# Performance work log

Hardware: AMD Instinct MI355X
Metric: run time of the kernel (lower is better)

Reference implementation:

```python
import jax, jax.numpy as jnp
import numpy as np

EMB = 1024
HEADS = 16
HEAD_DIM = EMB // HEADS
D_FF = 4 * EMB
EPS = 1e-5


def setup_inputs() -> dict:
    key = jax.random.key(0)
    ks = jax.random.split(key, 12)
    b, t = 4, 2048
    sc = 0.02
    return {
        "x": jax.random.normal(ks[0], (b, t, EMB), dtype=jnp.float32),
        # weights stored [in, out] (transpose of torch Linear.weight)
        "w_attn": jax.random.normal(ks[1], (EMB, 3 * EMB), dtype=jnp.float32) * sc,
        "b_attn": jnp.zeros((3 * EMB,), dtype=jnp.float32),
        "w_proj": jax.random.normal(ks[2], (EMB, EMB), dtype=jnp.float32) * sc,
        "b_proj": jnp.zeros((EMB,), dtype=jnp.float32),
        "ln1_g": jnp.ones((EMB,), dtype=jnp.float32),
        "ln1_b": jnp.zeros((EMB,), dtype=jnp.float32),
        "w_ff1": jax.random.normal(ks[3], (EMB, D_FF), dtype=jnp.float32) * sc,
        "b_ff1": jnp.zeros((D_FF,), dtype=jnp.float32),
        "w_ff2": jax.random.normal(ks[4], (D_FF, EMB), dtype=jnp.float32) * sc,
        "b_ff2": jnp.zeros((EMB,), dtype=jnp.float32),
        "ln2_g": jnp.ones((EMB,), dtype=jnp.float32),
        "ln2_b": jnp.zeros((EMB,), dtype=jnp.float32),
    }


def _layernorm(x, g, b):
    mu = jnp.mean(x, axis=-1, keepdims=True)
    var = jnp.var(x, axis=-1, keepdims=True)
    return (x - mu) * jax.lax.rsqrt(var + EPS) * g + b


def reference(x, w_attn, b_attn, w_proj, b_proj, ln1_g, ln1_b,
              w_ff1, b_ff1, w_ff2, b_ff2, ln2_g, ln2_b):
    b, t, e = x.shape
    h, s = HEADS, HEAD_DIM
    # fused qkv projection (GPT2-style c_attn)
    qkv = x @ w_attn + b_attn                      # [b, t, 3e]
    q, k, v = jnp.split(qkv, 3, axis=-1)
    q = q.reshape(b, t, h, s).transpose(0, 2, 1, 3)  # [b, h, t, s]
    k = k.reshape(b, t, h, s).transpose(0, 2, 1, 3)
    v = v.reshape(b, t, h, s).transpose(0, 2, 1, 3)
    dot = jnp.einsum('bhqs,bhks->bhqk', q, k) / jnp.sqrt(jnp.float32(s))
    # causal mask: mask_(..., mask_diagonal=False) zeroes i < j (strict upper)
    causal = jnp.tril(jnp.ones((t, t), dtype=bool))
    dot = jnp.where(causal, dot, jnp.float32(-jnp.inf))
    att = jax.nn.softmax(dot, axis=-1)
    out = jnp.einsum('bhqk,bhks->bhqs', att, v)    # [b, h, t, s]
    out = out.transpose(0, 2, 1, 3).reshape(b, t, e)
    attended = out @ w_proj + b_proj
    # residual + LayerNorm (dropout is identity in eval mode)
    x1 = _layernorm(attended + x, ln1_g, ln1_b)
    ff = jax.nn.relu(x1 @ w_ff1 + b_ff1) @ w_ff2 + b_ff2
    return _layernorm(ff + x1, ln2_g, ln2_b)
```

## Files before the change

### kernel.cpp

```cpp
#include <hip/hip_runtime.h>
#include <hip/hip_bf16.h>


typedef __attribute__((ext_vector_type(8))) short bf16x8;
typedef __attribute__((ext_vector_type(4))) float f32x4;

__device__ __forceinline__ float b2f(unsigned short u) {
  return __uint_as_float(((unsigned int)u) << 16);
}
__device__ __forceinline__ unsigned short f2b(float f) {
  unsigned int u = __float_as_uint(f);
  u += 0x7fffu + ((u >> 16) & 1u);
  return (unsigned short)(u >> 16);
}
__device__ __forceinline__ unsigned int pk2b(float a, float b) {
  __hip_bfloat162 h = __float22bfloat162_rn(make_float2(a, b));
  return *(unsigned int*)&h;
}
__device__ __forceinline__ void gload_lds16(const unsigned short* g, unsigned short* l) {
  __builtin_amdgcn_global_load_lds((const __attribute__((address_space(1))) void*)g,
                                   (__attribute__((address_space(3))) void*)l, 16, 0, 0);
}

__global__ __launch_bounds__(256) void cvt_bf16(const float* __restrict__ in,
                                                unsigned short* __restrict__ out, long n) {
  long i = ((long)blockIdx.x * 256 + threadIdx.x) * 4;
  if (i >= n) return;
  float4 v = *(const float4*)(in + i);
  *(ushort4*)(out + i) = make_ushort4(f2b(v.x), f2b(v.y), f2b(v.z), f2b(v.w));
}

__global__ __launch_bounds__(256) void transpose_bf16(const float* __restrict__ in,
                                                      unsigned short* __restrict__ out,
                                                      int R, int C) {
  __shared__ float tile[32][33];
  int c0 = blockIdx.x * 32, r0 = blockIdx.y * 32;
  for (int i = threadIdx.y; i < 32; i += 8)
    tile[i][threadIdx.x] = in[(long)(r0 + i) * C + c0 + threadIdx.x];
  __syncthreads();
  for (int i = threadIdx.y; i < 32; i += 8)
    out[(long)(c0 + i) * R + r0 + threadIdx.x] = f2b(tile[threadIdx.x][i]);
}

template <int EPI>
__global__ __launch_bounds__(256) void gemm_bf16(const unsigned short* __restrict__ A,
                                                 const unsigned short* __restrict__ Bt,
                                                 const float* __restrict__ bias,
                                                 void* __restrict__ Cout,
                                                 void* __restrict__ Cout2,
                                                 int M, int N, int K, int Kstride) {
  __shared__ unsigned short As[128 * 32];
  __shared__ unsigned short Bs[128 * 32];
  int t = threadIdx.x;
  int bm = blockIdx.x * 128, bn = blockIdx.y * 128;
  int chunk = blockIdx.z;
  int w = t >> 6, lane = t & 63;
  int wr = w >> 1, wc = w & 1, quad = lane >> 4, l16 = lane & 15;
  int srow = t >> 2, scol = (t & 3) * 8;

  const unsigned short* Ap = A + (long)(bm + srow) * Kstride + (long)chunk * K + scol;
  const unsigned short* Bp = Bt + (long)(bn + srow) * Kstride + (long)chunk * K + scol;
  unsigned short* Asw = As + w * 512;
  unsigned short* Bsw = Bs + w * 512;

  f32x4 acc[4][4] = {};

  for (int k0 = 0; k0 < K; k0 += 32) {
    __syncthreads();
    gload_lds16(Ap + k0, Asw);
    gload_lds16(Ap + (long)64 * Kstride + k0, Asw + 2048);
    gload_lds16(Bp + k0, Bsw);
    gload_lds16(Bp + (long)64 * Kstride + k0, Bsw + 2048);
    __syncthreads();
    bf16x8 af[4], bfr[4];
#pragma unroll
    for (int i = 0; i < 4; ++i)
      af[i] = *(const bf16x8*)(As + (wr * 64 + i * 16 + l16) * 32 + quad * 8);
#pragma unroll
    for (int j = 0; j < 4; ++j)
      bfr[j] = *(const bf16x8*)(Bs + (wc * 64 + j * 16 + l16) * 32 + quad * 8);
#pragma unroll
    for (int i = 0; i < 4; ++i)
#pragma unroll
      for (int j = 0; j < 4; ++j)
        acc[i][j] = __builtin_amdgcn_mfma_f32_16x16x32_bf16(af[i], bfr[j], acc[i][j], 0, 0, 0);
  }

  void* Cbase = chunk ? Cout2 : Cout;
#pragma unroll
  for (int i = 0; i < 4; ++i) {
#pragma unroll
    for (int j = 0; j < 4; ++j) {
      int gn = bn + wc * 64 + j * 16 + l16;
      float bv = chunk ? 0.f : bias[gn];
      if (EPI == 3 && gn >= 2048) {
        int h = (gn >> 6) & 15, s = gn & 63;
        int gm0 = bm + wr * 64 + i * 16 + quad * 4;
        int b = gm0 >> 11, tt0 = gm0 & 2047;
        unsigned short* vt = (unsigned short*)Cout + 16777216L;
        ushort4 us;
        us.x = f2b(acc[i][j][0] + bv);
        us.y = f2b(acc[i][j][1] + bv);
        us.z = f2b(acc[i][j][2] + bv);
        us.w = f2b(acc[i][j][3] + bv);
        *(ushort4*)(vt + (((long)(b * 16 + h)) * 64 + s) * 2048 + tt0) = us;
      } else {
#pragma unroll
        for (int r = 0; r < 4; ++r) {
          int gm = bm + wr * 64 + i * 16 + quad * 4 + r;
          float v = acc[i][j][r] + bv;
          if (EPI == 2) v = fmaxf(v, 0.f);
          if (EPI == 0) {
            ((float*)Cbase)[(long)gm * N + gn] = v;
          } else if (EPI == 1 || EPI == 2) {
            ((unsigned short*)Cbase)[(long)gm * N + gn] = f2b(v);
          } else {
            float sc = (gn < 1024) ? 0.18033688011112042f : 1.0f;
            ((unsigned short*)Cbase)[(long)gm * 2048 + gn] = f2b(v * sc);
          }
        }
      }
    }
  }
}

__global__ __launch_bounds__(256) void attn_mfma(const unsigned short* __restrict__ qkv,
                                                 unsigned short* __restrict__ outp) {
  const int LD = 72;
  __shared__ __align__(16) unsigned short Ks[64 * LD];
  __shared__ __align__(16) unsigned short Vts[64 * LD];
  __shared__ __align__(16) unsigned short Ps[4][16 * LD];
  int qa = blockIdx.x, qb = 31 - qa;
  int h = blockIdx.y, b = blockIdx.z;
  int t = threadIdx.x;
  int w = t >> 6, lane = t & 63, quad = lane >> 4, l16 = lane & 15;
  const unsigned short* qg = qkv + (long)(b * 2048) * 2048 + h * 64;
  const unsigned short* kg = qg + 1024;
  const unsigned short* vg = qkv + 16777216L + (((long)(b * 16 + h)) * 64) * 2048;
  unsigned short* Pw = &Ps[w][0];

  bf16x8 qfa[2], qfb[2];
#pragma unroll
  for (int ks = 0; ks < 2; ++ks) {
    qfa[ks] = *(const bf16x8*)(qg + (long)(qa * 64 + w * 16 + l16) * 2048 + ks * 32 + quad * 8);
    qfb[ks] = *(const bf16x8*)(qg + (long)(qb * 64 + w * 16 + l16) * 2048 + ks * 32 + quad * 8);
  }

  int sr = t >> 2, sc = (t & 3) * 16;
  const unsigned short* kp = kg + (long)sr * 2048 + sc;
  const unsigned short* vp = vg + (long)sr * 2048 + sc;
  int4 kv0 = *(const int4*)kp, kv1 = *(const int4*)(kp + 8);
  int4 vv0 = *(const int4*)vp, vv1 = *(const int4*)(vp + 8);
  kp += (long)64 * 2048;
  vp += 64;

  f32x4 oa[4] = {}, ob[4] = {};
  f32x4 la = {}, lb = {};
  const short ONE = 0x3F80;
  bf16x8 ones = {ONE, ONE, ONE, ONE, ONE, ONE, ONE, ONE};

  auto process = [&](const bf16x8* qf, int qt, int kt, f32x4* oacc, f32x4& lacc) {
    bool diag = (kt == qt);
#pragma unroll
    for (int rg = 0; rg < 4; ++rg) {
      bf16x8 kf0 = *(const bf16x8*)(Ks + (rg * 16 + l16) * LD + quad * 8);
      bf16x8 kf1 = *(const bf16x8*)(Ks + (rg * 16 + l16) * LD + 32 + quad * 8);
      f32x4 st = {};
      st = __builtin_amdgcn_mfma_f32_16x16x32_bf16(kf0, qf[0], st, 0, 0, 0);
      st = __builtin_amdgcn_mfma_f32_16x16x32_bf16(kf1, qf[1], st, 0, 0, 0);
      if (diag) {
        int kq = rg * 16 + quad * 4;
        int qq = w * 16 + l16;
#pragma unroll
        for (int r = 0; r < 4; ++r)
          if (kq + r > qq) st[r] = -1e30f;
      }
      unsigned int lo = pk2b(exp2f(st[0]), exp2f(st[1]));
      unsigned int hi = pk2b(exp2f(st[2]), exp2f(st[3]));
      *(uint2*)(Pw + l16 * LD + rg * 16 + quad * 4) = make_uint2(lo, hi);
    }
#pragma unroll
    for (int kc = 0; kc < 2; ++kc) {
      bf16x8 ap = *(const bf16x8*)(Pw + l16 * LD + kc * 32 + quad * 8);
      lacc = __builtin_amdgcn_mfma_f32_16x16x32_bf16(ap, ones, lacc, 0, 0, 0);
#pragma unroll
      for (int sg = 0; sg < 4; ++sg) {
        bf16x8 vf = *(const bf16x8*)(Vts + (sg * 16 + l16) * LD + kc * 32 + quad * 8);
        oacc[sg] = __builtin_amdgcn_mfma_f32_16x16x32_bf16(ap, vf, oacc[sg], 0, 0, 0);
      }
    }
  };

  for (int kt = 0; kt <= qb; ++kt) {
    __syncthreads();
    *(int4*)(Ks + sr * LD + sc) = kv0;
    *(int4*)(Ks + sr * LD + sc + 8) = kv1;
    *(int4*)(Vts + sr * LD + sc) = vv0;
    *(int4*)(Vts + sr * LD + sc + 8) = vv1;
    __syncthreads();
    if (kt < qb) {
      kv0 = *(const int4*)kp; kv1 = *(const int4*)(kp + 8);
      vv0 = *(const int4*)vp; vv1 = *(const int4*)(vp + 8);
      kp += (long)64 * 2048;
      vp += 64;
    }
    process(qfb, qb, kt, ob, lb);
    if (kt <= qa) process(qfa, qa, kt, oa, la);
  }

  auto epi = [&](int qt, f32x4* oacc, f32x4& lacc) {
#pragma unroll
    for (int r = 0; r < 4; ++r) {
      float invl = 1.f / lacc[r];
      int row = qt * 64 + w * 16 + quad * 4 + r;
      unsigned short* op = outp + ((long)(b * 2048 + row)) * 1024 + h * 64;
#pragma unroll
      for (int sg = 0; sg < 4; ++sg) op[sg * 16 + l16] = f2b(oacc[sg][r] * invl);
    }
  };
  epi(qa, oa, la);
  epi(qb, ob, lb);
}

__global__ __launch_bounds__(256) void ln_kernel(const float* __restrict__ a,
                                                 const float* __restrict__ a2,
                                                 const float* __restrict__ res,
                                                 const float* __restrict__ gam,
                                                 const float* __restrict__ bet,
                                                 float* __restrict__ outf,
                                                 unsigned short* __restrict__ outb) {
  int row = blockIdx.x, t = threadIdx.x;
  float4 av = *(const float4*)(a + (long)row * 1024 + t * 4);
  float4 rv = *(const float4*)(res + (long)row * 1024 + t * 4);
  float v0 = av.x + rv.x, v1 = av.y + rv.y, v2 = av.z + rv.z, v3 = av.w + rv.w;
  if (a2) {
    float4 a2v = *(const float4*)(a2 + (long)row * 1024 + t * 4);
    v0 += a2v.x; v1 += a2v.y; v2 += a2v.z; v3 += a2v.w;
  }
  float s = v0 + v1 + v2 + v3;
  float ss = v0 * v0 + v1 * v1 + v2 * v2 + v3 * v3;
#pragma unroll
  for (int off = 32; off >= 1; off >>= 1) {
    s += __shfl_down(s, off);
    ss += __shfl_down(ss, off);
  }
  __shared__ float sb[4], ssb[4];
  __shared__ float mean_s, inv_s;
  int w = t >> 6, lane = t & 63;
  if (lane == 0) { sb[w] = s; ssb[w] = ss; }
  __syncthreads();
  if (t == 0) {
    float S = sb[0] + sb[1] + sb[2] + sb[3];
    float SS = ssb[0] + ssb[1] + ssb[2] + ssb[3];
    float mean = S * (1.f / 1024.f);
    float var = SS * (1.f / 1024.f) - mean * mean;
    mean_s = mean;
    inv_s = rsqrtf(var + 1e-5f);
  }
  __syncthreads();
  float mean = mean_s, inv = inv_s;
  int c = t * 4;
  float4 gv = *(const float4*)(gam + c);
  float4 bv = *(const float4*)(bet + c);
  float y0 = (v0 - mean) * inv * gv.x + bv.x;
  float y1 = (v1 - mean) * inv * gv.y + bv.y;
  float y2 = (v2 - mean) * inv * gv.z + bv.z;
  float y3 = (v3 - mean) * inv * gv.w + bv.w;
  *(float4*)(outf + (long)row * 1024 + c) = make_float4(y0, y1, y2, y3);
  if (outb) {
    *(ushort4*)(outb + (long)row * 1024 + c) = make_ushort4(f2b(y0), f2b(y1), f2b(y2), f2b(y3));
  }
}

extern "C" void kernel_launch(void* const* d_in, const int* in_sizes, int n_in,
                              void* d_out, int out_size, void* d_ws, size_t ws_size,
                              hipStream_t stream) {
  const float* x      = (const float*)d_in[0];
  const float* w_attn = (const float*)d_in[1];
  const float* b_attn = (const float*)d_in[2];
  const float* w_proj = (const float*)d_in[3];
  const float* b_proj = (const float*)d_in[4];
  const float* ln1_g  = (const float*)d_in[5];
  const float* ln1_b  = (const float*)d_in[6];
  const float* w_ff1  = (const float*)d_in[7];
  const float* b_ff1  = (const float*)d_in[8];
  const float* w_ff2  = (const float*)d_in[9];
  const float* b_ff2  = (const float*)d_in[10];
  const float* ln2_g  = (const float*)d_in[11];
  const float* ln2_b  = (const float*)d_in[12];

  const long M = 8192, E = 1024;
  char* ws = (char*)d_ws;
  unsigned short* xb   = (unsigned short*)ws; ws += M * E * 2;
  unsigned short* wTa  = (unsigned short*)ws; ws += 3072L * 1024 * 2;
  unsigned short* wTp  = (unsigned short*)ws; ws += 1024L * 1024 * 2;
  unsigned short* wTf1 = (unsigned short*)ws; ws += 4096L * 1024 * 2;
  unsigned short* wTf2 = (unsigned short*)ws; ws += 4096L * 1024 * 2;
  unsigned short* qkvb = (unsigned short*)ws; ws += M * 3072 * 2;
  unsigned short* attb = (unsigned short*)ws; ws += M * E * 2;
  float* a1f = (float*)ws; ws += M * E * 4;
  float* x1f = (float*)ws; ws += M * E * 4;
  unsigned short* x1b = (unsigned short*)ws; ws += M * E * 2;
  unsigned short* hb = qkvb;
  float* f2 = a1f;
  float* prj1 = (float*)qkvb;
  float* ff21 = (float*)d_ws;

  cvt_bf16<<<dim3((M * E) / 4 / 256), dim3(256), 0, stream>>>(x, xb, M * E);
  transpose_bf16<<<dim3(3072 / 32, 1024 / 32), dim3(32, 8), 0, stream>>>(w_attn, wTa, 1024, 3072);
  transpose_bf16<<<dim3(1024 / 32, 1024 / 32), dim3(32, 8), 0, stream>>>(w_proj, wTp, 1024, 1024);
  transpose_bf16<<<dim3(4096 / 32, 1024 / 32), dim3(32, 8), 0, stream>>>(w_ff1, wTf1, 1024, 4096);
  transpose_bf16<<<dim3(1024 / 32, 4096 / 32), dim3(32, 8), 0, stream>>>(w_ff2, wTf2, 4096, 1024);
  gemm_bf16<3><<<dim3(64, 24, 1), dim3(256), 0, stream>>>(xb, wTa, b_attn, qkvb, nullptr, 8192, 3072, 1024, 1024);
  attn_mfma<<<dim3(16, 16, 4), dim3(256), 0, stream>>>(qkvb, attb);
  gemm_bf16<0><<<dim3(64, 8, 2), dim3(256), 0, stream>>>(attb, wTp, b_proj, a1f, prj1, 8192, 1024, 512, 1024);
  ln_kernel<<<dim3(8192), dim3(256), 0, stream>>>(a1f, prj1, x, ln1_g, ln1_b, x1f, x1b);
  gemm_bf16<2><<<dim3(64, 32, 1), dim3(256), 0, stream>>>(x1b, wTf1, b_ff1, hb, nullptr, 8192, 4096, 1024, 1024);
  gemm_bf16<0><<<dim3(64, 8, 2), dim3(256), 0, stream>>>(hb, wTf2, b_ff2, f2, ff21, 8192, 1024, 2048, 4096);
  ln_kernel<<<dim3(8192), dim3(256), 0, stream>>>(f2, ff21, x1f, ln2_g, ln2_b, (float*)d_out, nullptr);
}
```

Measured before the change: 607.4 us.

## Replace GEMM with 256x256-tile, 4-stage pipelined, LDS-swizzled kernel

Replaces the 128x128 single-buffered bf16 GEMM with a 512-thread kernel that computes 256x256 tiles. It uses a 4-deep LDS ring with global_load_lds prefetch three stages ahead and explicit vmcnt waits, plus an XOR swizzle on LDS columns to reduce bank conflicts. It also adds a block-id remap for L2 locality and raises wave priority around the MFMA loop. Larger tiles raise data reuse and hide global-load latency, but use 128KB of LDS per block, give fewer blocks per GEMM, and rely on hand-tuned wait counts.

```diff
diff --git a/kernel.cpp b/kernel.cpp
--- a/kernel.cpp
+++ b/kernel.cpp
@@ -5,9 +5,6 @@
 typedef __attribute__((ext_vector_type(8))) short bf16x8;
 typedef __attribute__((ext_vector_type(4))) float f32x4;
 
-__device__ __forceinline__ float b2f(unsigned short u) {
-  return __uint_as_float(((unsigned int)u) << 16);
-}
 __device__ __forceinline__ unsigned short f2b(float f) {
   unsigned int u = __float_as_uint(f);
   u += 0x7fffu + ((u >> 16) & 1u);
@@ -43,59 +40,90 @@
 }
 
 template <int EPI>
-__global__ __launch_bounds__(256) void gemm_bf16(const unsigned short* __restrict__ A,
-                                                 const unsigned short* __restrict__ Bt,
-                                                 const float* __restrict__ bias,
-                                                 void* __restrict__ Cout,
-                                                 void* __restrict__ Cout2,
-                                                 int M, int N, int K, int Kstride) {
-  __shared__ unsigned short As[128 * 32];
-  __shared__ unsigned short Bs[128 * 32];
-  int t = threadIdx.x;
-  int bm = blockIdx.x * 128, bn = blockIdx.y * 128;
-  int chunk = blockIdx.z;
-  int w = t >> 6, lane = t & 63;
-  int wr = w >> 1, wc = w & 1, quad = lane >> 4, l16 = lane & 15;
-  int srow = t >> 2, scol = (t & 3) * 8;
-
-  const unsigned short* Ap = A + (long)(bm + srow) * Kstride + (long)chunk * K + scol;
-  const unsigned short* Bp = Bt + (long)(bn + srow) * Kstride + (long)chunk * K + scol;
-  unsigned short* Asw = As + w * 512;
-  unsigned short* Bsw = Bs + w * 512;
-
-  f32x4 acc[4][4] = {};
-
-  for (int k0 = 0; k0 < K; k0 += 32) {
-    __syncthreads();
-    gload_lds16(Ap + k0, Asw);
-    gload_lds16(Ap + (long)64 * Kstride + k0, Asw + 2048);
-    gload_lds16(Bp + k0, Bsw);
-    gload_lds16(Bp + (long)64 * Kstride + k0, Bsw + 2048);
-    __syncthreads();
-    bf16x8 af[4], bfr[4];
-#pragma unroll
-    for (int i = 0; i < 4; ++i)
-      af[i] = *(const bf16x8*)(As + (wr * 64 + i * 16 + l16) * 32 + quad * 8);
+__global__ __launch_bounds__(512, 2) void gemm256(const unsigned short* __restrict__ A,
+                                                  const unsigned short* __restrict__ Bt,
+                                                  const float* __restrict__ bias,
+                                                  void* __restrict__ Cout,
+                                                  void* __restrict__ Cout2,
+                                                  int N, int K, int Kstride) {
+  __shared__ __align__(16) unsigned short As[4][256 * 32];
+  __shared__ __align__(16) unsigned short Bs[4][256 * 32];
+
+  int tid = threadIdx.x;
+  int wv = tid >> 6, lane = tid & 63, quad = lane >> 4, l16 = lane & 15;
+  int wm = wv >> 2, wn = wv & 3;
+
+  int nwg = gridDim.x, id = blockIdx.x;
+  int sid = (id & 7) * (nwg >> 3) + (id >> 3);
+  int bm256 = (sid & 31) * 256, bn256 = (sid >> 5) * 256;
+  int chunk = blockIdx.y;
+  long kbase = (long)chunk * K;
+
+  int row1 = tid >> 2, row2 = row1 + 128;
+  long dsl = ((tid & 3) ^ ((tid >> 3) & 3)) * 8;
+  const unsigned short* Ap1 = A + (long)(bm256 + row1) * Kstride + kbase + dsl;
+  const unsigned short* Ap2 = A + (long)(bm256 + row2) * Kstride + kbase + dsl;
+  const unsigned short* Bp1 = Bt + (long)(bn256 + row1) * Kstride + kbase + dsl;
+  const unsigned short* Bp2 = Bt + (long)(bn256 + row2) * Kstride + kbase + dsl;
+  int ldsoff1 = wv * 512, ldsoff2 = wv * 512 + 4096;
+
+  auto stage = [&](int t) {
+    int buf = t & 3;
+    long ko = (long)t * 32;
+    gload_lds16(Ap1 + ko, &As[buf][ldsoff1]);
+    gload_lds16(Ap2 + ko, &As[buf][ldsoff2]);
+    gload_lds16(Bp1 + ko, &Bs[buf][ldsoff1]);
+    gload_lds16(Bp2 + ko, &Bs[buf][ldsoff2]);
+  };
+
+  f32x4 acc[8][4] = {};
+  int sl8 = (quad ^ ((l16 >> 1) & 3)) * 8;
+  int arow = wm * 128 + l16;
+  int brow = wn * 64 + l16;
+
+  int NT = K >> 5;
+  stage(0); stage(1); stage(2);
+  asm volatile("s_waitcnt vmcnt(8)\n\ts_barrier" ::: "memory");
+  __builtin_amdgcn_sched_barrier(0);
+
+  for (int t = 0; t < NT; ++t) {
+    if (t + 3 < NT) stage(t + 3);
+    __builtin_amdgcn_sched_barrier(0);
+    const unsigned short* Ab = &As[t & 3][0];
+    const unsigned short* Bb = &Bs[t & 3][0];
+    bf16x8 af[8], bfr[4];
+#pragma unroll
+    for (int i = 0; i < 8; ++i)
+      af[i] = *(const bf16x8*)(Ab + (arow + i * 16) * 32 + sl8);
 #pragma unroll
     for (int j = 0; j < 4; ++j)
-      bfr[j] = *(const bf16x8*)(Bs + (wc * 64 + j * 16 + l16) * 32 + quad * 8);
-#pragma unroll
-    for (int i = 0; i < 4; ++i)
+      bfr[j] = *(const bf16x8*)(Bb + (brow + j * 16) * 32 + sl8);
+    __builtin_amdgcn_s_setprio(1);
+#pragma unroll
+    for (int i = 0; i < 8; ++i)
 #pragma unroll
       for (int j = 0; j < 4; ++j)
         acc[i][j] = __builtin_amdgcn_mfma_f32_16x16x32_bf16(af[i], bfr[j], acc[i][j], 0, 0, 0);
+    __builtin_amdgcn_s_setprio(0);
+    __builtin_amdgcn_sched_barrier(0);
+    if (t + 1 < NT) {
+      if (t + 3 < NT)       asm volatile("s_waitcnt vmcnt(8)\n\ts_barrier" ::: "memory");
+      else if (t + 3 == NT) asm volatile("s_waitcnt vmcnt(4)\n\ts_barrier" ::: "memory");
+      else                  asm volatile("s_waitcnt vmcnt(0)\n\ts_barrier" ::: "memory");
+      __builtin_amdgcn_sched_barrier(0);
+    }
   }
 
   void* Cbase = chunk ? Cout2 : Cout;
 #pragma unroll
-  for (int i = 0; i < 4; ++i) {
+  for (int i = 0; i < 8; ++i) {
 #pragma unroll
     for (int j = 0; j < 4; ++j) {
-      int gn = bn + wc * 64 + j * 16 + l16;
+      int gn = bn256 + wn * 64 + j * 16 + l16;
       float bv = chunk ? 0.f : bias[gn];
       if (EPI == 3 && gn >= 2048) {
         int h = (gn >> 6) & 15, s = gn & 63;
-        int gm0 = bm + wr * 64 + i * 16 + quad * 4;
+        int gm0 = bm256 + wm * 128 + i * 16 + quad * 4;
         int b = gm0 >> 11, tt0 = gm0 & 2047;
         unsigned short* vt = (unsigned short*)Cout + 16777216L;
         ushort4 us;
@@ -107,12 +135,12 @@
       } else {
 #pragma unroll
         for (int r = 0; r < 4; ++r) {
-          int gm = bm + wr * 64 + i * 16 + quad * 4 + r;
+          int gm = bm256 + wm * 128 + i * 16 + quad * 4 + r;
           float v = acc[i][j][r] + bv;
           if (EPI == 2) v = fmaxf(v, 0.f);
           if (EPI == 0) {
             ((float*)Cbase)[(long)gm * N + gn] = v;
-          } else if (EPI == 1 || EPI == 2) {
+          } else if (EPI == 2) {
             ((unsigned short*)Cbase)[(long)gm * N + gn] = f2b(v);
           } else {
             float sc = (gn < 1024) ? 0.18033688011112042f : 1.0f;
@@ -311,11 +339,11 @@
   transpose_bf16<<<dim3(1024 / 32, 1024 / 32), dim3(32, 8), 0, stream>>>(w_proj, wTp, 1024, 1024);
   transpose_bf16<<<dim3(4096 / 32, 1024 / 32), dim3(32, 8), 0, stream>>>(w_ff1, wTf1, 1024, 4096);
   transpose_bf16<<<dim3(1024 / 32, 4096 / 32), dim3(32, 8), 0, stream>>>(w_ff2, wTf2, 4096, 1024);
-  gemm_bf16<3><<<dim3(64, 24, 1), dim3(256), 0, stream>>>(xb, wTa, b_attn, qkvb, nullptr, 8192, 3072, 1024, 1024);
+  gemm256<3><<<dim3(384, 1), dim3(512), 0, stream>>>(xb, wTa, b_attn, qkvb, nullptr, 3072, 1024, 1024);
   attn_mfma<<<dim3(16, 16, 4), dim3(256), 0, stream>>>(qkvb, attb);
-  gemm_bf16<0><<<dim3(64, 8, 2), dim3(256), 0, stream>>>(attb, wTp, b_proj, a1f, prj1, 8192, 1024, 512, 1024);
+  gemm256<0><<<dim3(128, 2), dim3(512), 0, stream>>>(attb, wTp, b_proj, a1f, prj1, 1024, 512, 1024);
   ln_kernel<<<dim3(8192), dim3(256), 0, stream>>>(a1f, prj1, x, ln1_g, ln1_b, x1f, x1b);
-  gemm_bf16<2><<<dim3(64, 32, 1), dim3(256), 0, stream>>>(x1b, wTf1, b_ff1, hb, nullptr, 8192, 4096, 1024, 1024);
-  gemm_bf16<0><<<dim3(64, 8, 2), dim3(256), 0, stream>>>(hb, wTf2, b_ff2, f2, ff21, 8192, 1024, 2048, 4096);
+  gemm256<2><<<dim3(512, 1), dim3(512), 0, stream>>>(x1b, wTf1, b_ff1, hb, nullptr, 4096, 1024, 1024);
+  gemm256<0><<<dim3(128, 2), dim3(512), 0, stream>>>(hb, wTf2, b_ff2, f2, ff21, 1024, 2048, 4096);
   ln_kernel<<<dim3(8192), dim3(256), 0, stream>>>(f2, ff21, x1f, ln2_g, ln2_b, (float*)d_out, nullptr);
 }
```

New measurement: 602.0 us. About the same (-0.9%).
